# Kernel optimization log

Measured on AMD Instinct MI355X. Metric: run time of the kernel, lower is better.

Reference implementation:

```python
import jax, jax.numpy as jnp
import numpy as np

TOP_K = 2


def setup_inputs() -> dict:
    key = jax.random.key(0)
    k0, k1, k2, k3, k4 = jax.random.split(key, 5)
    B, S, H, F, E = 2, 1024, 2048, 7168, 8
    scale = 0.02
    return {
        "hidden_states": jax.random.normal(k0, (B, S, H), jnp.float32),
        "Wg": jax.random.normal(k1, (E, H), jnp.float32) * scale,
        "w1": jax.random.normal(k2, (E, F, H), jnp.float32) * scale,
        "w3": jax.random.normal(k3, (E, F, H), jnp.float32) * scale,
        "w2": jax.random.normal(k4, (E, H, F), jnp.float32) * scale,
    }


def reference(hidden_states, Wg, w1, w3, w2):
    B, S, H = hidden_states.shape
    E = Wg.shape[0]
    x = hidden_states.reshape(-1, H)                      # [T, H]
    T = x.shape[0]

    # Router: logits -> softmax (float32) -> top-k -> renormalize
    router_logits = jnp.einsum("th,eh->te", x, Wg)        # [T, E]
    probs = jax.nn.softmax(router_logits.astype(jnp.float32), axis=-1)
    top_w, top_idx = jax.lax.top_k(probs, TOP_K)          # [T, K]
    top_w = top_w / jnp.sum(top_w, axis=-1, keepdims=True)
    top_w = top_w.astype(x.dtype)

    # Combine weights: [T, E], zero for unselected experts
    combine = jnp.zeros((T, E), x.dtype).at[
        jnp.arange(T)[:, None], top_idx
    ].add(top_w)

    out = jnp.zeros((T, H), x.dtype)
    for e in range(E):
        h = jax.nn.silu(x @ w1[e].T) * (x @ w3[e].T)      # [T, F]
        out = out + (h @ w2[e].T) * combine[:, e:e + 1]   # [T, H]

    return out.reshape(B, S, H), router_logits
```

## Files before the change

### kernel.cpp

```cpp
#include <hip/hip_runtime.h>

#define T_TOK 2048
#define H_DIM 2048
#define F_DIM 7168
#define E_NUM 8
#define MAX_SLOTS 5120
#define N13 (2 * F_DIM)

typedef __attribute__((ext_vector_type(8))) _Float16 f16x8;
typedef __attribute__((ext_vector_type(4))) float    f32x4;

#define GLL(g, l) __builtin_amdgcn_global_load_lds(                          \
    (const __attribute__((address_space(1))) void*)(g),                      \
    (__attribute__((address_space(3))) void*)(l), 16, 0, 0)


__global__ __launch_bounds__(256) void cvt13_kernel(const float* __restrict__ w1,
                                                    const float* __restrict__ w3,
                                                    _Float16* __restrict__ w13h) {
    int b = blockIdx.x;
    int e = b / N13;
    int c = b - e * N13;
    int blk = c >> 6, sub = c & 63;
    int f = blk * 32 + (sub & 31);
    const float* src = (sub < 32 ? w1 : w3) + ((size_t)e * F_DIM + f) * H_DIM + threadIdx.x * 8;
    _Float16* dst = w13h + (size_t)b * H_DIM + threadIdx.x * 8;
    float4 a = *(const float4*)src;
    float4 bb = *(const float4*)(src + 4);
    f16x8 h;
    h[0]=(_Float16)a.x;  h[1]=(_Float16)a.y;  h[2]=(_Float16)a.z;  h[3]=(_Float16)a.w;
    h[4]=(_Float16)bb.x; h[5]=(_Float16)bb.y; h[6]=(_Float16)bb.z; h[7]=(_Float16)bb.w;
    *(f16x8*)dst = h;
}

__global__ __launch_bounds__(256) void cvtw_kernel(const float* __restrict__ src,
                                                   _Float16* __restrict__ dst) {
    size_t i = ((size_t)blockIdx.x * 256 + threadIdx.x) * 8;
    float4 a = *(const float4*)(src + i);
    float4 b = *(const float4*)(src + i + 4);
    f16x8 h;
    h[0]=(_Float16)a.x; h[1]=(_Float16)a.y; h[2]=(_Float16)a.z; h[3]=(_Float16)a.w;
    h[4]=(_Float16)b.x; h[5]=(_Float16)b.y; h[6]=(_Float16)b.z; h[7]=(_Float16)b.w;
    *(f16x8*)(dst + i) = h;
}


__global__ __launch_bounds__(256) void router_kernel(
    const float* __restrict__ x, const float* __restrict__ wg,
    float* __restrict__ logits_out, int* __restrict__ tk_e,
    float* __restrict__ tk_w, int* __restrict__ meta) {
    int wave = threadIdx.x >> 6;
    int lane = threadIdx.x & 63;
    int t = blockIdx.x * 4 + wave;
    const float* xr = x + (size_t)t * H_DIM;

    float xv[32];
#pragma unroll
    for (int i = 0; i < 8; i++) {
        float4 v = *(const float4*)(xr + i * 256 + lane * 4);
        xv[i*4+0] = v.x; xv[i*4+1] = v.y; xv[i*4+2] = v.z; xv[i*4+3] = v.w;
    }
    float lg[E_NUM];
#pragma unroll
    for (int e = 0; e < E_NUM; e++) {
        const float* wr = wg + (size_t)e * H_DIM;
        float acc = 0.f;
#pragma unroll
        for (int i = 0; i < 8; i++) {
            float4 v = *(const float4*)(wr + i * 256 + lane * 4);
            acc += xv[i*4+0]*v.x + xv[i*4+1]*v.y + xv[i*4+2]*v.z + xv[i*4+3]*v.w;
        }
#pragma unroll
        for (int s = 32; s > 0; s >>= 1) acc += __shfl_xor(acc, s, 64);
        lg[e] = acc;
    }
    if (lane == 0) {
        float b0 = -3e38f, b1 = -3e38f; int i0 = 0, i1 = 0;
#pragma unroll
        for (int e = 0; e < E_NUM; e++) {
            float le = lg[e];
            if (le > b0)      { b1 = b0; i1 = i0; b0 = le; i0 = e; }
            else if (le > b1) { b1 = le; i1 = e; }
        }
        float w0 = 1.f / (1.f + __expf(b1 - b0));
        float w1v = 1.f - w0;
#pragma unroll
        for (int e = 0; e < E_NUM; e++) logits_out[(size_t)t * E_NUM + e] = lg[e];
        tk_e[t*2+0] = i0; tk_w[t*2+0] = w0;
        tk_e[t*2+1] = i1; tk_w[t*2+1] = w1v;
        atomicAdd(&meta[i0], 1);
        atomicAdd(&meta[i1], 1);
    }
}

__global__ void scan_kernel(int* __restrict__ meta, int* __restrict__ slot_tok,
                            float* __restrict__ slot_w) {
    int lane = threadIdx.x;
    int cnts[E_NUM], pads[E_NUM], bases[E_NUM];
    int run = 0;
#pragma unroll
    for (int e = 0; e < E_NUM; e++) {
        cnts[e] = meta[e];
        pads[e] = (cnts[e] + 127) & ~127;
        bases[e] = run;
        run += pads[e];
    }
    if (lane < E_NUM) { meta[8 + lane] = pads[lane]; meta[16 + lane] = bases[lane]; }
    for (int e = 0; e < E_NUM; e++)
        for (int i = cnts[e] + lane; i < pads[e]; i += 64) {
            slot_tok[bases[e] + i] = 0;
            slot_w[bases[e] + i] = 0.f;
        }
}

__global__ __launch_bounds__(256) void assign_kernel(
    const int* __restrict__ tk_e, const float* __restrict__ tk_w,
    int* __restrict__ meta, int* __restrict__ slot_tok, float* __restrict__ slot_w) {
    int t = blockIdx.x * 256 + threadIdx.x;
    if (t >= T_TOK) return;
#pragma unroll
    for (int k = 0; k < 2; k++) {
        int e = tk_e[t*2+k];
        int pos = atomicAdd(&meta[24 + e], 1);
        int s = meta[16 + e] + pos;
        slot_tok[s] = t;
        slot_w[s] = tk_w[t*2+k];
    }
}

__global__ __launch_bounds__(512, 2) void ffn1_kernel(
    const _Float16* __restrict__ xb, const _Float16* __restrict__ w13h,
    const int* __restrict__ slot_tok, const int* __restrict__ meta,
    _Float16* __restrict__ hbuf) {
    int e = blockIdx.z;
    int cntpad = meta[8 + e];
    int mb = blockIdx.y;
    if (mb * 256 >= cntpad) return;
    int base = meta[16 + e];
    int nb = blockIdx.x;

    __shared__ _Float16 sA[2][256][64];
    __shared__ _Float16 sB[2][256][64];

    int tid  = threadIdx.x;
    int lane = tid & 63;
    int wave = tid >> 6;
    int wm = wave >> 2, wn = wave & 3;
    int w8 = wave * 8;

    int lr = lane & 15;
    int sw = lane & 7;
    int sg = lane >> 4;
    int offk0 = lr * 64 + ((sg    ) ^ sw) * 8;
    int offk1 = lr * 64 + ((sg + 4) ^ sw) * 8;

    int rsub = lane >> 3;
    int sl   = (lane & 7) ^ rsub;
    int slot0 = base + mb * 256;

    const _Float16* aG[4];
    const _Float16* bG[4];
#pragma unroll
    for (int q = 0; q < 4; q++) {
        int r = mb * 256 + q * 64 + w8 + rsub;
        int tok = (r < cntpad) ? slot_tok[base + r] : 0;
        aG[q] = xb + (size_t)tok * H_DIM + sl * 8;
        bG[q] = w13h + ((size_t)e * N13 + (size_t)nb * 256 + q * 64 + w8 + rsub) * H_DIM + sl * 8;
    }

    f32x4 zero = {0.f, 0.f, 0.f, 0.f};
    f32x4 acc[8][4];
#pragma unroll
    for (int m = 0; m < 8; m++)
#pragma unroll
        for (int n = 0; n < 4; n++) acc[m][n] = zero;

    const int NT = H_DIM / 64;
#pragma unroll
    for (int q = 0; q < 4; q++) GLL(aG[q] + 0,  &sA[0][q*64 + w8][0]);
#pragma unroll
    for (int q = 0; q < 4; q++) GLL(bG[q] + 0,  &sB[0][q*64 + w8][0]);
#pragma unroll
    for (int q = 0; q < 4; q++) GLL(aG[q] + 64, &sA[1][q*64 + w8][0]);
#pragma unroll
    for (int q = 0; q < 4; q++) GLL(bG[q] + 64, &sB[1][q*64 + w8][0]);

    for (int t = 0; t < NT; ++t) {
        if (t < NT - 1) asm volatile("s_waitcnt vmcnt(8)" ::: "memory");
        else            asm volatile("s_waitcnt vmcnt(0)" ::: "memory");
        __builtin_amdgcn_sched_barrier(0);
        __builtin_amdgcn_s_barrier();
        __builtin_amdgcn_sched_barrier(0);
        int bd = t & 1;
        const _Float16* Ab = &sA[bd][wm * 128][0];
        const _Float16* Bb = &sB[bd][wn * 64][0];
        f16x8 bf[2][4];
#pragma unroll
        for (int n = 0; n < 4; n++) {
            bf[0][n] = *(const f16x8*)(const void*)(Bb + n * 1024 + offk0);
            bf[1][n] = *(const f16x8*)(const void*)(Bb + n * 1024 + offk1);
        }
        __builtin_amdgcn_s_setprio(1);
#pragma unroll
        for (int m = 0; m < 8; m++) {
            f16x8 a0 = *(const f16x8*)(const void*)(Ab + m * 1024 + offk0);
            f16x8 a1 = *(const f16x8*)(const void*)(Ab + m * 1024 + offk1);
#pragma unroll
            for (int n = 0; n < 4; n++) {
                acc[m][n] = __builtin_amdgcn_mfma_f32_16x16x32_f16(a0, bf[0][n], acc[m][n], 0, 0, 0);
                acc[m][n] = __builtin_amdgcn_mfma_f32_16x16x32_f16(a1, bf[1][n], acc[m][n], 0, 0, 0);
            }
        }
        __builtin_amdgcn_s_setprio(0);
        __builtin_amdgcn_sched_barrier(0);
        __builtin_amdgcn_s_barrier();
        __builtin_amdgcn_sched_barrier(0);
        if (t + 2 < NT) {
            int k2 = (t + 2) * 64;
#pragma unroll
            for (int q = 0; q < 4; q++) GLL(aG[q] + k2, &sA[bd][q*64 + w8][0]);
#pragma unroll
            for (int q = 0; q < 4; q++) GLL(bG[q] + k2, &sB[bd][q*64 + w8][0]);
        }
    }

    int row_e0 = mb * 256 + wm * 128;
    int fb = nb * 128 + wn * 32;
#pragma unroll
    for (int m = 0; m < 8; m++) {
#pragma unroll
        for (int j = 0; j < 4; j++) {
            int re = row_e0 + m * 16 + (lane >> 4) * 4 + j;
            if (re < cntpad) {
                size_t srow = (size_t)(base + re) * F_DIM;
#pragma unroll
                for (int n = 0; n < 2; n++) {
                    float a1 = acc[m][n][j], a3 = acc[m][n + 2][j];
                    float hv = a1 * a3 / (1.f + __expf(-a1));
                    hbuf[srow + fb + n * 16 + lr] = (_Float16)hv;
                }
            }
        }
    }
}

__global__ __launch_bounds__(512, 2) void ffn2_kernel(
    const _Float16* __restrict__ hbuf, const _Float16* __restrict__ w2h,
    const int* __restrict__ slot_tok, const float* __restrict__ slot_w,
    const int* __restrict__ meta, float* __restrict__ out) {
    int e = blockIdx.z;
    int cntpad = meta[8 + e];
    int mb = blockIdx.y;
    if (mb * 128 >= cntpad) return;
    int base = meta[16 + e];
    int nb = blockIdx.x;

    __shared__ _Float16 sA[2][128][64];
    __shared__ _Float16 sB[2][256][64];

    int tid  = threadIdx.x;
    int lane = tid & 63;
    int wave = tid >> 6;
    int wm = wave >> 2, wn = wave & 3;
    int w8 = wave * 8;

    int lr = lane & 15;
    int sw = lane & 7;
    int sg = lane >> 4;
    int offk0 = lr * 64 + ((sg    ) ^ sw) * 8;
    int offk1 = lr * 64 + ((sg + 4) ^ sw) * 8;

    int rsub = lane >> 3;
    int sl   = (lane & 7) ^ rsub;
    int slot0 = base + mb * 128;

    const _Float16* aG[2];
    const _Float16* bG[4];
#pragma unroll
    for (int q = 0; q < 2; q++)
        aG[q] = hbuf + (size_t)(slot0 + q * 64 + w8 + rsub) * F_DIM + sl * 8;
#pragma unroll
    for (int q = 0; q < 4; q++)
        bG[q] = w2h + ((size_t)e * H_DIM + (size_t)nb * 256 + q * 64 + w8 + rsub) * F_DIM + sl * 8;

    f32x4 zero = {0.f, 0.f, 0.f, 0.f};
    f32x4 acc[4][4];
#pragma unroll
    for (int m = 0; m < 4; m++)
#pragma unroll
        for (int n = 0; n < 4; n++) acc[m][n] = zero;

    const int NT = F_DIM / 64;
#pragma unroll
    for (int q = 0; q < 2; q++) GLL(aG[q] + 0,  &sA[0][q*64 + w8][0]);
#pragma unroll
    for (int q = 0; q < 4; q++) GLL(bG[q] + 0,  &sB[0][q*64 + w8][0]);
#pragma unroll
    for (int q = 0; q < 2; q++) GLL(aG[q] + 64, &sA[1][q*64 + w8][0]);
#pragma unroll
    for (int q = 0; q < 4; q++) GLL(bG[q] + 64, &sB[1][q*64 + w8][0]);

    for (int t = 0; t < NT; ++t) {
        if (t < NT - 1) asm volatile("s_waitcnt vmcnt(6)" ::: "memory");
        else            asm volatile("s_waitcnt vmcnt(0)" ::: "memory");
        __builtin_amdgcn_sched_barrier(0);
        __builtin_amdgcn_s_barrier();
        __builtin_amdgcn_sched_barrier(0);
        int bd = t & 1;
        const _Float16* Ab = &sA[bd][wm * 64][0];
        const _Float16* Bb = &sB[bd][wn * 64][0];
        f16x8 bf[2][4];
#pragma unroll
        for (int n = 0; n < 4; n++) {
            bf[0][n] = *(const f16x8*)(const void*)(Bb + n * 1024 + offk0);
            bf[1][n] = *(const f16x8*)(const void*)(Bb + n * 1024 + offk1);
        }
        __builtin_amdgcn_s_setprio(1);
#pragma unroll
        for (int m = 0; m < 4; m++) {
            f16x8 a0 = *(const f16x8*)(const void*)(Ab + m * 1024 + offk0);
            f16x8 a1 = *(const f16x8*)(const void*)(Ab + m * 1024 + offk1);
#pragma unroll
            for (int n = 0; n < 4; n++) {
                acc[m][n] = __builtin_amdgcn_mfma_f32_16x16x32_f16(a0, bf[0][n], acc[m][n], 0, 0, 0);
                acc[m][n] = __builtin_amdgcn_mfma_f32_16x16x32_f16(a1, bf[1][n], acc[m][n], 0, 0, 0);
            }
        }
        __builtin_amdgcn_s_setprio(0);
        __builtin_amdgcn_sched_barrier(0);
        __builtin_amdgcn_s_barrier();
        __builtin_amdgcn_sched_barrier(0);
        if (t + 2 < NT) {
            int k2 = (t + 2) * 64;
#pragma unroll
            for (int q = 0; q < 2; q++) GLL(aG[q] + k2, &sA[bd][q*64 + w8][0]);
#pragma unroll
            for (int q = 0; q < 4; q++) GLL(bG[q] + k2, &sB[bd][q*64 + w8][0]);
        }
    }

    int row0 = mb * 128 + wm * 64;
    int col0 = nb * 256 + wn * 64;
#pragma unroll
    for (int m = 0; m < 4; m++) {
        int rb = row0 + m * 16 + (lane >> 4) * 4;
        int toks[4]; float wts[4];
#pragma unroll
        for (int j = 0; j < 4; j++) {
            int s = base + rb + j;
            toks[j] = slot_tok[s];
            wts[j]  = slot_w[s];
        }
#pragma unroll
        for (int n = 0; n < 4; n++) {
            int col = col0 + n * 16 + lr;
            f32x4 v = acc[m][n];
#pragma unroll
            for (int j = 0; j < 4; j++)
                atomicAdd(&out[(size_t)toks[j] * H_DIM + col], v[j] * wts[j]);
        }
    }
}

extern "C" void kernel_launch(void* const* d_in, const int* in_sizes, int n_in,
                              void* d_out, int out_size, void* d_ws, size_t ws_size,
                              hipStream_t stream) {
    const float* x  = (const float*)d_in[0];
    const float* wg = (const float*)d_in[1];
    const float* w1 = (const float*)d_in[2];
    const float* w3 = (const float*)d_in[3];
    const float* w2 = (const float*)d_in[4];
    float* out = (float*)d_out;
    float* logits = out + (size_t)T_TOK * H_DIM;

    const size_t WELEM = (size_t)E_NUM * F_DIM * H_DIM;

    char* ws = (char*)d_ws;
    _Float16* w13h = (_Float16*)ws;
    _Float16* w2h  = w13h + 2 * WELEM;
    _Float16* hbuf = w2h + WELEM;
    _Float16* xb   = hbuf + (size_t)MAX_SLOTS * F_DIM;
    char* p = (char*)(xb + (size_t)T_TOK * H_DIM);
    int*   slot_tok = (int*)p;   p += MAX_SLOTS * 4;
    float* slot_w   = (float*)p; p += MAX_SLOTS * 4;
    int*   tk_e     = (int*)p;   p += T_TOK * 2 * 4;
    float* tk_w     = (float*)p; p += T_TOK * 2 * 4;
    int*   meta     = (int*)p;

    hipMemsetAsync(d_out, 0, (size_t)out_size * sizeof(float), stream);
    hipMemsetAsync(meta, 0, 32 * sizeof(int), stream);

    cvt13_kernel<<<dim3(E_NUM * N13), 256, 0, stream>>>(w1, w3, w13h);
    cvtw_kernel<<<dim3(WELEM / (256 * 8)), 256, 0, stream>>>(w2, w2h);
    cvtw_kernel<<<dim3((size_t)T_TOK * H_DIM / (256 * 8)), 256, 0, stream>>>(x, xb);

    router_kernel<<<dim3(T_TOK / 4), 256, 0, stream>>>(x, wg, logits, tk_e, tk_w, meta);
    scan_kernel<<<dim3(1), 64, 0, stream>>>(meta, slot_tok, slot_w);
    assign_kernel<<<dim3(T_TOK / 256), 256, 0, stream>>>(tk_e, tk_w, meta, slot_tok, slot_w);

    ffn1_kernel<<<dim3(N13 / 256, 8, E_NUM), 512, 0, stream>>>(xb, w13h, slot_tok, meta, hbuf);
    ffn2_kernel<<<dim3(H_DIM / 256, 16, E_NUM), 512, 0, stream>>>(hbuf, w2h, slot_tok, slot_w, meta, out);
}
```

Baseline: 1.292 ms.

## Fuse fp32 weight conversion into FFN GEMM loads, drop separate conversion passes

Removes the standalone kernels that convert w1/w3/w2 to fp16 in workspace. The FFN GEMMs now read fp32 weights straight from global memory into registers, convert them, and write them to swizzled shared memory, so the weight-conversion round trip through HBM goes away. Tiles shrink to 128x128 with 256-thread blocks, single-buffered shared memory, and register prefetch of the next weight tile. The cost is that each weight tile is read in fp32 by every M-block of an expert, which doubles weight bytes per read, and the kernels lose the earlier double-buffered LDS pipeline.

```diff
diff --git a/kernel.cpp b/kernel.cpp
--- a/kernel.cpp
+++ b/kernel.cpp
@@ -5,7 +5,6 @@
 #define F_DIM 7168
 #define E_NUM 8
 #define MAX_SLOTS 5120
-#define N13 (2 * F_DIM)
 
 typedef __attribute__((ext_vector_type(8))) _Float16 f16x8;
 typedef __attribute__((ext_vector_type(4))) float    f32x4;
@@ -15,25 +14,7 @@
     (__attribute__((address_space(3))) void*)(l), 16, 0, 0)
 
 
-__global__ __launch_bounds__(256) void cvt13_kernel(const float* __restrict__ w1,
-                                                    const float* __restrict__ w3,
-                                                    _Float16* __restrict__ w13h) {
-    int b = blockIdx.x;
-    int e = b / N13;
-    int c = b - e * N13;
-    int blk = c >> 6, sub = c & 63;
-    int f = blk * 32 + (sub & 31);
-    const float* src = (sub < 32 ? w1 : w3) + ((size_t)e * F_DIM + f) * H_DIM + threadIdx.x * 8;
-    _Float16* dst = w13h + (size_t)b * H_DIM + threadIdx.x * 8;
-    float4 a = *(const float4*)src;
-    float4 bb = *(const float4*)(src + 4);
-    f16x8 h;
-    h[0]=(_Float16)a.x;  h[1]=(_Float16)a.y;  h[2]=(_Float16)a.z;  h[3]=(_Float16)a.w;
-    h[4]=(_Float16)bb.x; h[5]=(_Float16)bb.y; h[6]=(_Float16)bb.z; h[7]=(_Float16)bb.w;
-    *(f16x8*)dst = h;
-}
-
-__global__ __launch_bounds__(256) void cvtw_kernel(const float* __restrict__ src,
+__global__ __launch_bounds__(256) void cvtx_kernel(const float* __restrict__ src,
                                                    _Float16* __restrict__ dst) {
     size_t i = ((size_t)blockIdx.x * 256 + threadIdx.x) * 8;
     float4 a = *(const float4*)(src + i);
@@ -44,7 +25,6 @@
     *(f16x8*)(dst + i) = h;
 }
 
-
 __global__ __launch_bounds__(256) void router_kernel(
     const float* __restrict__ x, const float* __restrict__ wg,
     float* __restrict__ logits_out, int* __restrict__ tk_e,
@@ -128,124 +108,125 @@
     }
 }
 
-__global__ __launch_bounds__(512, 2) void ffn1_kernel(
-    const _Float16* __restrict__ xb, const _Float16* __restrict__ w13h,
-    const int* __restrict__ slot_tok, const int* __restrict__ meta,
-    _Float16* __restrict__ hbuf) {
+__global__ __launch_bounds__(256, 4) void ffn1_kernel(
+    const _Float16* __restrict__ xb, const float* __restrict__ w1,
+    const float* __restrict__ w3, const int* __restrict__ slot_tok,
+    const int* __restrict__ meta, _Float16* __restrict__ hbuf) {
     int e = blockIdx.z;
     int cntpad = meta[8 + e];
     int mb = blockIdx.y;
-    if (mb * 256 >= cntpad) return;
+    if (mb * 128 >= cntpad) return;
     int base = meta[16 + e];
     int nb = blockIdx.x;
 
-    __shared__ _Float16 sA[2][256][64];
-    __shared__ _Float16 sB[2][256][64];
+    __shared__ _Float16 sA[128][64];
+    __shared__ _Float16 sB[128][64];
+    char* sAc = (char*)&sA[0][0];
+    char* sBc = (char*)&sB[0][0];
 
     int tid  = threadIdx.x;
     int lane = tid & 63;
     int wave = tid >> 6;
-    int wm = wave >> 2, wn = wave & 3;
-    int w8 = wave * 8;
-
     int lr = lane & 15;
-    int sw = lane & 7;
     int sg = lane >> 4;
-    int offk0 = lr * 64 + ((sg    ) ^ sw) * 8;
-    int offk1 = lr * 64 + ((sg + 4) ^ sw) * 8;
+    int sw7 = lane & 7;
+    int bro0 = ((sg    ) ^ sw7) * 16;
+    int bro1 = ((sg + 4) ^ sw7) * 16;
 
     int rsub = lane >> 3;
-    int sl   = (lane & 7) ^ rsub;
-    int slot0 = base + mb * 256;
-
+    int sl = (lane & 7) ^ rsub;
     const _Float16* aG[4];
-    const _Float16* bG[4];
 #pragma unroll
     for (int q = 0; q < 4; q++) {
-        int r = mb * 256 + q * 64 + w8 + rsub;
-        int tok = (r < cntpad) ? slot_tok[base + r] : 0;
+        int row = mb * 128 + wave * 32 + q * 8 + rsub;
+        int tok = slot_tok[base + row];
         aG[q] = xb + (size_t)tok * H_DIM + sl * 8;
-        bG[q] = w13h + ((size_t)e * N13 + (size_t)nb * 256 + q * 64 + w8 + rsub) * H_DIM + sl * 8;
-    }
+    }
+
+    int brow = wave * 32 + (lane >> 1);
+    const float* wsel = (brow < 64) ? w1 : w3;
+    const float* bsrc = wsel + ((size_t)e * F_DIM + (size_t)nb * 64 + (brow & 63)) * H_DIM
+                        + (lane & 1) * 32;
+    int bwr[4];
+#pragma unroll
+    for (int q = 0; q < 4; q++)
+        bwr[q] = brow * 128 + ((((lane & 1) * 4 + q) ^ (brow & 7)) * 16);
 
     f32x4 zero = {0.f, 0.f, 0.f, 0.f};
-    f32x4 acc[8][4];
-#pragma unroll
-    for (int m = 0; m < 8; m++)
-#pragma unroll
-        for (int n = 0; n < 4; n++) acc[m][n] = zero;
+    f32x4 acc[2][8];
+#pragma unroll
+    for (int m = 0; m < 2; m++)
+#pragma unroll
+        for (int n = 0; n < 8; n++) acc[m][n] = zero;
 
     const int NT = H_DIM / 64;
-#pragma unroll
-    for (int q = 0; q < 4; q++) GLL(aG[q] + 0,  &sA[0][q*64 + w8][0]);
-#pragma unroll
-    for (int q = 0; q < 4; q++) GLL(bG[q] + 0,  &sB[0][q*64 + w8][0]);
-#pragma unroll
-    for (int q = 0; q < 4; q++) GLL(aG[q] + 64, &sA[1][q*64 + w8][0]);
-#pragma unroll
-    for (int q = 0; q < 4; q++) GLL(bG[q] + 64, &sB[1][q*64 + w8][0]);
+    float4 br[8];
+#pragma unroll
+    for (int q = 0; q < 8; q++) br[q] = *(const float4*)(bsrc + q * 4);
 
     for (int t = 0; t < NT; ++t) {
-        if (t < NT - 1) asm volatile("s_waitcnt vmcnt(8)" ::: "memory");
-        else            asm volatile("s_waitcnt vmcnt(0)" ::: "memory");
+        int k = t * 64;
         __builtin_amdgcn_sched_barrier(0);
         __builtin_amdgcn_s_barrier();
         __builtin_amdgcn_sched_barrier(0);
-        int bd = t & 1;
-        const _Float16* Ab = &sA[bd][wm * 128][0];
-        const _Float16* Bb = &sB[bd][wn * 64][0];
-        f16x8 bf[2][4];
-#pragma unroll
-        for (int n = 0; n < 4; n++) {
-            bf[0][n] = *(const f16x8*)(const void*)(Bb + n * 1024 + offk0);
-            bf[1][n] = *(const f16x8*)(const void*)(Bb + n * 1024 + offk1);
-        }
+#pragma unroll
+        for (int q = 0; q < 4; q++) {
+            float4 a = br[2*q], b = br[2*q+1];
+            f16x8 p;
+            p[0]=(_Float16)a.x; p[1]=(_Float16)a.y; p[2]=(_Float16)a.z; p[3]=(_Float16)a.w;
+            p[4]=(_Float16)b.x; p[5]=(_Float16)b.y; p[6]=(_Float16)b.z; p[7]=(_Float16)b.w;
+            *(f16x8*)(sBc + bwr[q]) = p;
+        }
+#pragma unroll
+        for (int q = 0; q < 4; q++) GLL(aG[q] + k, &sA[wave * 32 + q * 8][0]);
+        if (t + 1 < NT) {
+#pragma unroll
+            for (int q = 0; q < 8; q++) br[q] = *(const float4*)(bsrc + k + 64 + q * 4);
+            asm volatile("s_waitcnt vmcnt(8) lgkmcnt(0)" ::: "memory");
+        } else {
+            asm volatile("s_waitcnt vmcnt(0) lgkmcnt(0)" ::: "memory");
+        }
+        __builtin_amdgcn_sched_barrier(0);
+        __builtin_amdgcn_s_barrier();
+        __builtin_amdgcn_sched_barrier(0);
         __builtin_amdgcn_s_setprio(1);
 #pragma unroll
-        for (int m = 0; m < 8; m++) {
-            f16x8 a0 = *(const f16x8*)(const void*)(Ab + m * 1024 + offk0);
-            f16x8 a1 = *(const f16x8*)(const void*)(Ab + m * 1024 + offk1);
+        for (int ks = 0; ks < 2; ks++) {
+            int bro = ks ? bro1 : bro0;
+            f16x8 bf[8];
+#pragma unroll
+            for (int n = 0; n < 8; n++)
+                bf[n] = *(const f16x8*)(sBc + (n * 16 + lr) * 128 + bro);
+#pragma unroll
+            for (int m = 0; m < 2; m++) {
+                f16x8 av = *(const f16x8*)(sAc + (wave * 32 + m * 16 + lr) * 128 + bro);
+#pragma unroll
+                for (int n = 0; n < 8; n++)
+                    acc[m][n] = __builtin_amdgcn_mfma_f32_16x16x32_f16(av, bf[n], acc[m][n], 0, 0, 0);
+            }
+        }
+        __builtin_amdgcn_s_setprio(0);
+    }
+
+    int fb = nb * 64;
+#pragma unroll
+    for (int m = 0; m < 2; m++) {
+#pragma unroll
+        for (int j = 0; j < 4; j++) {
+            int row = mb * 128 + wave * 32 + m * 16 + sg * 4 + j;
+            size_t srow = (size_t)(base + row) * F_DIM;
 #pragma unroll
             for (int n = 0; n < 4; n++) {
-                acc[m][n] = __builtin_amdgcn_mfma_f32_16x16x32_f16(a0, bf[0][n], acc[m][n], 0, 0, 0);
-                acc[m][n] = __builtin_amdgcn_mfma_f32_16x16x32_f16(a1, bf[1][n], acc[m][n], 0, 0, 0);
+                float a1 = acc[m][n][j], a3 = acc[m][n + 4][j];
+                float hv = a1 * a3 / (1.f + __expf(-a1));
+                hbuf[srow + fb + n * 16 + lr] = (_Float16)hv;
             }
         }
-        __builtin_amdgcn_s_setprio(0);
-        __builtin_amdgcn_sched_barrier(0);
-        __builtin_amdgcn_s_barrier();
-        __builtin_amdgcn_sched_barrier(0);
-        if (t + 2 < NT) {
-            int k2 = (t + 2) * 64;
-#pragma unroll
-            for (int q = 0; q < 4; q++) GLL(aG[q] + k2, &sA[bd][q*64 + w8][0]);
-#pragma unroll
-            for (int q = 0; q < 4; q++) GLL(bG[q] + k2, &sB[bd][q*64 + w8][0]);
-        }
-    }
-
-    int row_e0 = mb * 256 + wm * 128;
-    int fb = nb * 128 + wn * 32;
-#pragma unroll
-    for (int m = 0; m < 8; m++) {
-#pragma unroll
-        for (int j = 0; j < 4; j++) {
-            int re = row_e0 + m * 16 + (lane >> 4) * 4 + j;
-            if (re < cntpad) {
-                size_t srow = (size_t)(base + re) * F_DIM;
-#pragma unroll
-                for (int n = 0; n < 2; n++) {
-                    float a1 = acc[m][n][j], a3 = acc[m][n + 2][j];
-                    float hv = a1 * a3 / (1.f + __expf(-a1));
-                    hbuf[srow + fb + n * 16 + lr] = (_Float16)hv;
-                }
-            }
-        }
-    }
-}
-
-__global__ __launch_bounds__(512, 2) void ffn2_kernel(
-    const _Float16* __restrict__ hbuf, const _Float16* __restrict__ w2h,
+    }
+}
+
+__global__ __launch_bounds__(256, 4) void ffn2_kernel(
+    const _Float16* __restrict__ hbuf, const float* __restrict__ w2,
     const int* __restrict__ slot_tok, const float* __restrict__ slot_w,
     const int* __restrict__ meta, float* __restrict__ out) {
     int e = blockIdx.z;
@@ -255,33 +236,36 @@
     int base = meta[16 + e];
     int nb = blockIdx.x;
 
-    __shared__ _Float16 sA[2][128][64];
-    __shared__ _Float16 sB[2][256][64];
+    __shared__ _Float16 sA[128][64];
+    __shared__ _Float16 sB[128][64];
+    char* sAc = (char*)&sA[0][0];
+    char* sBc = (char*)&sB[0][0];
 
     int tid  = threadIdx.x;
     int lane = tid & 63;
     int wave = tid >> 6;
-    int wm = wave >> 2, wn = wave & 3;
-    int w8 = wave * 8;
-
+    int wm = wave >> 1, wn = wave & 1;
     int lr = lane & 15;
-    int sw = lane & 7;
     int sg = lane >> 4;
-    int offk0 = lr * 64 + ((sg    ) ^ sw) * 8;
-    int offk1 = lr * 64 + ((sg + 4) ^ sw) * 8;
+    int sw7 = lane & 7;
+    int bro0 = ((sg    ) ^ sw7) * 16;
+    int bro1 = ((sg + 4) ^ sw7) * 16;
 
     int rsub = lane >> 3;
-    int sl   = (lane & 7) ^ rsub;
+    int sl = (lane & 7) ^ rsub;
     int slot0 = base + mb * 128;
-
-    const _Float16* aG[2];
-    const _Float16* bG[4];
-#pragma unroll
-    for (int q = 0; q < 2; q++)
-        aG[q] = hbuf + (size_t)(slot0 + q * 64 + w8 + rsub) * F_DIM + sl * 8;
+    const _Float16* aG[4];
 #pragma unroll
     for (int q = 0; q < 4; q++)
-        bG[q] = w2h + ((size_t)e * H_DIM + (size_t)nb * 256 + q * 64 + w8 + rsub) * F_DIM + sl * 8;
+        aG[q] = hbuf + (size_t)(slot0 + wave * 32 + q * 8 + rsub) * F_DIM + sl * 8;
+
+    int brow = wave * 32 + (lane >> 1);
+    const float* bsrc = w2 + ((size_t)e * H_DIM + (size_t)nb * 128 + brow) * F_DIM
+                        + (lane & 1) * 32;
+    int bwr[4];
+#pragma unroll
+    for (int q = 0; q < 4; q++)
+        bwr[q] = brow * 128 + ((((lane & 1) * 4 + q) ^ (brow & 7)) * 16);
 
     f32x4 zero = {0.f, 0.f, 0.f, 0.f};
     f32x4 acc[4][4];
@@ -291,59 +275,59 @@
         for (int n = 0; n < 4; n++) acc[m][n] = zero;
 
     const int NT = F_DIM / 64;
-#pragma unroll
-    for (int q = 0; q < 2; q++) GLL(aG[q] + 0,  &sA[0][q*64 + w8][0]);
-#pragma unroll
-    for (int q = 0; q < 4; q++) GLL(bG[q] + 0,  &sB[0][q*64 + w8][0]);
-#pragma unroll
-    for (int q = 0; q < 2; q++) GLL(aG[q] + 64, &sA[1][q*64 + w8][0]);
-#pragma unroll
-    for (int q = 0; q < 4; q++) GLL(bG[q] + 64, &sB[1][q*64 + w8][0]);
+    float4 br[8];
+#pragma unroll
+    for (int q = 0; q < 8; q++) br[q] = *(const float4*)(bsrc + q * 4);
 
     for (int t = 0; t < NT; ++t) {
-        if (t < NT - 1) asm volatile("s_waitcnt vmcnt(6)" ::: "memory");
-        else            asm volatile("s_waitcnt vmcnt(0)" ::: "memory");
+        int k = t * 64;
         __builtin_amdgcn_sched_barrier(0);
         __builtin_amdgcn_s_barrier();
         __builtin_amdgcn_sched_barrier(0);
-        int bd = t & 1;
-        const _Float16* Ab = &sA[bd][wm * 64][0];
-        const _Float16* Bb = &sB[bd][wn * 64][0];
-        f16x8 bf[2][4];
-#pragma unroll
-        for (int n = 0; n < 4; n++) {
-            bf[0][n] = *(const f16x8*)(const void*)(Bb + n * 1024 + offk0);
-            bf[1][n] = *(const f16x8*)(const void*)(Bb + n * 1024 + offk1);
-        }
+#pragma unroll
+        for (int q = 0; q < 4; q++) {
+            float4 a = br[2*q], b = br[2*q+1];
+            f16x8 p;
+            p[0]=(_Float16)a.x; p[1]=(_Float16)a.y; p[2]=(_Float16)a.z; p[3]=(_Float16)a.w;
+            p[4]=(_Float16)b.x; p[5]=(_Float16)b.y; p[6]=(_Float16)b.z; p[7]=(_Float16)b.w;
+            *(f16x8*)(sBc + bwr[q]) = p;
+        }
+#pragma unroll
+        for (int q = 0; q < 4; q++) GLL(aG[q] + k, &sA[wave * 32 + q * 8][0]);
+        if (t + 1 < NT) {
+#pragma unroll
+            for (int q = 0; q < 8; q++) br[q] = *(const float4*)(bsrc + k + 64 + q * 4);
+            asm volatile("s_waitcnt vmcnt(8) lgkmcnt(0)" ::: "memory");
+        } else {
+            asm volatile("s_waitcnt vmcnt(0) lgkmcnt(0)" ::: "memory");
+        }
+        __builtin_amdgcn_sched_barrier(0);
+        __builtin_amdgcn_s_barrier();
+        __builtin_amdgcn_sched_barrier(0);
         __builtin_amdgcn_s_setprio(1);
 #pragma unroll
-        for (int m = 0; m < 4; m++) {
-            f16x8 a0 = *(const f16x8*)(const void*)(Ab + m * 1024 + offk0);
-            f16x8 a1 = *(const f16x8*)(const void*)(Ab + m * 1024 + offk1);
-#pragma unroll
-            for (int n = 0; n < 4; n++) {
-                acc[m][n] = __builtin_amdgcn_mfma_f32_16x16x32_f16(a0, bf[0][n], acc[m][n], 0, 0, 0);
-                acc[m][n] = __builtin_amdgcn_mfma_f32_16x16x32_f16(a1, bf[1][n], acc[m][n], 0, 0, 0);
+        for (int ks = 0; ks < 2; ks++) {
+            int bro = ks ? bro1 : bro0;
+            f16x8 bf[4];
+#pragma unroll
+            for (int n = 0; n < 4; n++)
+                bf[n] = *(const f16x8*)(sBc + ((wn * 64 + n * 16 + lr) * 128) + bro);
+#pragma unroll
+            for (int m = 0; m < 4; m++) {
+                f16x8 av = *(const f16x8*)(sAc + ((wm * 64 + m * 16 + lr) * 128) + bro);
+#pragma unroll
+                for (int n = 0; n < 4; n++)
+                    acc[m][n] = __builtin_amdgcn_mfma_f32_16x16x32_f16(av, bf[n], acc[m][n], 0, 0, 0);
             }
         }
         __builtin_amdgcn_s_setprio(0);
-        __builtin_amdgcn_sched_barrier(0);
-        __builtin_amdgcn_s_barrier();
-        __builtin_amdgcn_sched_barrier(0);
-        if (t + 2 < NT) {
-            int k2 = (t + 2) * 64;
-#pragma unroll
-            for (int q = 0; q < 2; q++) GLL(aG[q] + k2, &sA[bd][q*64 + w8][0]);
-#pragma unroll
-            for (int q = 0; q < 4; q++) GLL(bG[q] + k2, &sB[bd][q*64 + w8][0]);
-        }
     }
 
     int row0 = mb * 128 + wm * 64;
-    int col0 = nb * 256 + wn * 64;
+    int col0 = nb * 128 + wn * 64;
 #pragma unroll
     for (int m = 0; m < 4; m++) {
-        int rb = row0 + m * 16 + (lane >> 4) * 4;
+        int rb = row0 + m * 16 + sg * 4;
         int toks[4]; float wts[4];
 #pragma unroll
         for (int j = 0; j < 4; j++) {
@@ -373,12 +357,8 @@
     float* out = (float*)d_out;
     float* logits = out + (size_t)T_TOK * H_DIM;
 
-    const size_t WELEM = (size_t)E_NUM * F_DIM * H_DIM;
-
     char* ws = (char*)d_ws;
-    _Float16* w13h = (_Float16*)ws;
-    _Float16* w2h  = w13h + 2 * WELEM;
-    _Float16* hbuf = w2h + WELEM;
+    _Float16* hbuf = (_Float16*)ws;
     _Float16* xb   = hbuf + (size_t)MAX_SLOTS * F_DIM;
     char* p = (char*)(xb + (size_t)T_TOK * H_DIM);
     int*   slot_tok = (int*)p;   p += MAX_SLOTS * 4;
@@ -390,14 +370,11 @@
     hipMemsetAsync(d_out, 0, (size_t)out_size * sizeof(float), stream);
     hipMemsetAsync(meta, 0, 32 * sizeof(int), stream);
 
-    cvt13_kernel<<<dim3(E_NUM * N13), 256, 0, stream>>>(w1, w3, w13h);
-    cvtw_kernel<<<dim3(WELEM / (256 * 8)), 256, 0, stream>>>(w2, w2h);
-    cvtw_kernel<<<dim3((size_t)T_TOK * H_DIM / (256 * 8)), 256, 0, stream>>>(x, xb);
-
+    cvtx_kernel<<<dim3((size_t)T_TOK * H_DIM / (256 * 8)), 256, 0, stream>>>(x, xb);
     router_kernel<<<dim3(T_TOK / 4), 256, 0, stream>>>(x, wg, logits, tk_e, tk_w, meta);
     scan_kernel<<<dim3(1), 64, 0, stream>>>(meta, slot_tok, slot_w);
     assign_kernel<<<dim3(T_TOK / 256), 256, 0, stream>>>(tk_e, tk_w, meta, slot_tok, slot_w);
 
-    ffn1_kernel<<<dim3(N13 / 256, 8, E_NUM), 512, 0, stream>>>(xb, w13h, slot_tok, meta, hbuf);
-    ffn2_kernel<<<dim3(H_DIM / 256, 16, E_NUM), 512, 0, stream>>>(hbuf, w2h, slot_tok, slot_w, meta, out);
-}
+    ffn1_kernel<<<dim3(F_DIM / 64, 16, E_NUM), 256, 0, stream>>>(xb, w1, w3, slot_tok, meta, hbuf);
+    ffn2_kernel<<<dim3(H_DIM / 128, 16, E_NUM), 256, 0, stream>>>(hbuf, w2, slot_tok, slot_w, meta, out);
+}
```

Result: slower. 4.829 ms (+273.9%).

## Triple-buffer LDS and split K-steps into interleaved load/MFMA phases in FFN GEMMs

Applied to the files above, without the earlier changes.

Both FFN GEMM kernels move from double to triple-buffered LDS and split each 64-wide K tile into two half-steps. Global-to-LDS loads for tile t+2 are spread across the two half-steps, interleaved with LDS reads and MFMA bursts. FFN1 also shrinks its M tile from 256 to 128 rows, doubling the grid's M blocks and halving accumulator registers. The cost is extra barriers per iteration and more LDS per block (about 144KB), which can limit how many blocks fit on a CU.

```diff
diff --git a/kernel.cpp b/kernel.cpp
--- a/kernel.cpp
+++ b/kernel.cpp
@@ -135,110 +135,131 @@
     int e = blockIdx.z;
     int cntpad = meta[8 + e];
     int mb = blockIdx.y;
-    if (mb * 256 >= cntpad) return;
+    if (mb * 128 >= cntpad) return;
     int base = meta[16 + e];
     int nb = blockIdx.x;
 
-    __shared__ _Float16 sA[2][256][64];
-    __shared__ _Float16 sB[2][256][64];
+    __shared__ _Float16 sA[3][128][64];
+    __shared__ _Float16 sB[3][256][64];
 
     int tid  = threadIdx.x;
     int lane = tid & 63;
     int wave = tid >> 6;
     int wm = wave >> 2, wn = wave & 3;
     int w8 = wave * 8;
-
     int lr = lane & 15;
-    int sw = lane & 7;
     int sg = lane >> 4;
-    int offk0 = lr * 64 + ((sg    ) ^ sw) * 8;
-    int offk1 = lr * 64 + ((sg + 4) ^ sw) * 8;
+    int sw7 = lane & 7;
+    int so0 = ((sg    ) ^ sw7) * 8;
+    int so1 = ((sg + 4) ^ sw7) * 8;
+    int rb  = lr * 64;
 
     int rsub = lane >> 3;
-    int sl   = (lane & 7) ^ rsub;
-    int slot0 = base + mb * 256;
-
-    const _Float16* aG[4];
+    int sl   = sw7 ^ rsub;
+    const _Float16* aG[2];
+#pragma unroll
+    for (int q = 0; q < 2; q++) {
+        int row = q * 64 + w8 + rsub;
+        int tok = slot_tok[base + mb * 128 + row];
+        aG[q] = xb + (size_t)tok * H_DIM + sl * 8;
+    }
     const _Float16* bG[4];
 #pragma unroll
-    for (int q = 0; q < 4; q++) {
-        int r = mb * 256 + q * 64 + w8 + rsub;
-        int tok = (r < cntpad) ? slot_tok[base + r] : 0;
-        aG[q] = xb + (size_t)tok * H_DIM + sl * 8;
+    for (int q = 0; q < 4; q++)
         bG[q] = w13h + ((size_t)e * N13 + (size_t)nb * 256 + q * 64 + w8 + rsub) * H_DIM + sl * 8;
-    }
 
     f32x4 zero = {0.f, 0.f, 0.f, 0.f};
-    f32x4 acc[8][4];
-#pragma unroll
-    for (int m = 0; m < 8; m++)
+    f32x4 acc[4][4];
+#pragma unroll
+    for (int m = 0; m < 4; m++)
 #pragma unroll
         for (int n = 0; n < 4; n++) acc[m][n] = zero;
 
     const int NT = H_DIM / 64;
-#pragma unroll
-    for (int q = 0; q < 4; q++) GLL(aG[q] + 0,  &sA[0][q*64 + w8][0]);
-#pragma unroll
-    for (int q = 0; q < 4; q++) GLL(bG[q] + 0,  &sB[0][q*64 + w8][0]);
-#pragma unroll
-    for (int q = 0; q < 4; q++) GLL(aG[q] + 64, &sA[1][q*64 + w8][0]);
-#pragma unroll
-    for (int q = 0; q < 4; q++) GLL(bG[q] + 64, &sB[1][q*64 + w8][0]);
+
+#pragma unroll
+    for (int t0 = 0; t0 < 2; t0++) {
+        int k = t0 * 64;
+        GLL(aG[0] + k, &sA[t0][w8][0]);
+        GLL(aG[1] + k, &sA[t0][64 + w8][0]);
+#pragma unroll
+        for (int q = 0; q < 4; q++) GLL(bG[q] + k, &sB[t0][q * 64 + w8][0]);
+    }
+    asm volatile("s_waitcnt vmcnt(6)" ::: "memory");
+    __builtin_amdgcn_sched_barrier(0);
+    __builtin_amdgcn_s_barrier();
+    __builtin_amdgcn_sched_barrier(0);
 
     for (int t = 0; t < NT; ++t) {
-        if (t < NT - 1) asm volatile("s_waitcnt vmcnt(8)" ::: "memory");
+        int r  = t % 3;
+        int r2 = (t + 2) % 3;
+        int k2 = (t + 2) * 64;
+        const _Float16* Ab = &sA[r][wm * 64][0];
+        const _Float16* Bb = &sB[r][wn * 64][0];
+
+        f16x8 a0[4], b0[4];
+#pragma unroll
+        for (int n = 0; n < 4; n++) b0[n] = *(const f16x8*)(const void*)(Bb + n * 1024 + rb + so0);
+#pragma unroll
+        for (int m = 0; m < 4; m++) a0[m] = *(const f16x8*)(const void*)(Ab + m * 1024 + rb + so0);
+        if (t + 2 < NT) {
+            GLL(aG[0] + k2, &sA[r2][w8][0]);
+            GLL(aG[1] + k2, &sA[r2][64 + w8][0]);
+            GLL(bG[0] + k2, &sB[r2][w8][0]);
+        }
+        __builtin_amdgcn_sched_barrier(0);
+        __builtin_amdgcn_s_barrier();
+        __builtin_amdgcn_sched_barrier(0);
+        __builtin_amdgcn_s_setprio(1);
+#pragma unroll
+        for (int m = 0; m < 4; m++)
+#pragma unroll
+            for (int n = 0; n < 4; n++)
+                acc[m][n] = __builtin_amdgcn_mfma_f32_16x16x32_f16(a0[m], b0[n], acc[m][n], 0, 0, 0);
+        __builtin_amdgcn_s_setprio(0);
+        __builtin_amdgcn_sched_barrier(0);
+        __builtin_amdgcn_s_barrier();
+        __builtin_amdgcn_sched_barrier(0);
+
+        f16x8 a1[4], b1[4];
+#pragma unroll
+        for (int n = 0; n < 4; n++) b1[n] = *(const f16x8*)(const void*)(Bb + n * 1024 + rb + so1);
+#pragma unroll
+        for (int m = 0; m < 4; m++) a1[m] = *(const f16x8*)(const void*)(Ab + m * 1024 + rb + so1);
+        if (t + 2 < NT) {
+            GLL(bG[1] + k2, &sB[r2][64 + w8][0]);
+            GLL(bG[2] + k2, &sB[r2][128 + w8][0]);
+            GLL(bG[3] + k2, &sB[r2][192 + w8][0]);
+        }
+        if (t < NT - 2) asm volatile("s_waitcnt vmcnt(6)" ::: "memory");
         else            asm volatile("s_waitcnt vmcnt(0)" ::: "memory");
         __builtin_amdgcn_sched_barrier(0);
         __builtin_amdgcn_s_barrier();
         __builtin_amdgcn_sched_barrier(0);
-        int bd = t & 1;
-        const _Float16* Ab = &sA[bd][wm * 128][0];
-        const _Float16* Bb = &sB[bd][wn * 64][0];
-        f16x8 bf[2][4];
-#pragma unroll
-        for (int n = 0; n < 4; n++) {
-            bf[0][n] = *(const f16x8*)(const void*)(Bb + n * 1024 + offk0);
-            bf[1][n] = *(const f16x8*)(const void*)(Bb + n * 1024 + offk1);
-        }
         __builtin_amdgcn_s_setprio(1);
 #pragma unroll
-        for (int m = 0; m < 8; m++) {
-            f16x8 a0 = *(const f16x8*)(const void*)(Ab + m * 1024 + offk0);
-            f16x8 a1 = *(const f16x8*)(const void*)(Ab + m * 1024 + offk1);
-#pragma unroll
-            for (int n = 0; n < 4; n++) {
-                acc[m][n] = __builtin_amdgcn_mfma_f32_16x16x32_f16(a0, bf[0][n], acc[m][n], 0, 0, 0);
-                acc[m][n] = __builtin_amdgcn_mfma_f32_16x16x32_f16(a1, bf[1][n], acc[m][n], 0, 0, 0);
-            }
-        }
+        for (int m = 0; m < 4; m++)
+#pragma unroll
+            for (int n = 0; n < 4; n++)
+                acc[m][n] = __builtin_amdgcn_mfma_f32_16x16x32_f16(a1[m], b1[n], acc[m][n], 0, 0, 0);
         __builtin_amdgcn_s_setprio(0);
         __builtin_amdgcn_sched_barrier(0);
         __builtin_amdgcn_s_barrier();
         __builtin_amdgcn_sched_barrier(0);
-        if (t + 2 < NT) {
-            int k2 = (t + 2) * 64;
-#pragma unroll
-            for (int q = 0; q < 4; q++) GLL(aG[q] + k2, &sA[bd][q*64 + w8][0]);
-#pragma unroll
-            for (int q = 0; q < 4; q++) GLL(bG[q] + k2, &sB[bd][q*64 + w8][0]);
-        }
-    }
-
-    int row_e0 = mb * 256 + wm * 128;
-    int fb = nb * 128 + wn * 32;
-#pragma unroll
-    for (int m = 0; m < 8; m++) {
+    }
+
+    int fb = (nb * 4 + wn) * 32;
+#pragma unroll
+    for (int m = 0; m < 4; m++) {
 #pragma unroll
         for (int j = 0; j < 4; j++) {
-            int re = row_e0 + m * 16 + (lane >> 4) * 4 + j;
-            if (re < cntpad) {
-                size_t srow = (size_t)(base + re) * F_DIM;
-#pragma unroll
-                for (int n = 0; n < 2; n++) {
-                    float a1 = acc[m][n][j], a3 = acc[m][n + 2][j];
-                    float hv = a1 * a3 / (1.f + __expf(-a1));
-                    hbuf[srow + fb + n * 16 + lr] = (_Float16)hv;
-                }
+            int re = mb * 128 + wm * 64 + m * 16 + sg * 4 + j;
+            size_t srow = (size_t)(base + re) * F_DIM;
+#pragma unroll
+            for (int n = 0; n < 2; n++) {
+                float a1v = acc[m][n][j], a3v = acc[m][n + 2][j];
+                float hv = a1v * a3v / (1.f + __expf(-a1v));
+                hbuf[srow + fb + n * 16 + lr] = (_Float16)hv;
             }
         }
     }
@@ -255,30 +276,28 @@
     int base = meta[16 + e];
     int nb = blockIdx.x;
 
-    __shared__ _Float16 sA[2][128][64];
-    __shared__ _Float16 sB[2][256][64];
+    __shared__ _Float16 sA[3][128][64];
+    __shared__ _Float16 sB[3][256][64];
 
     int tid  = threadIdx.x;
     int lane = tid & 63;
     int wave = tid >> 6;
     int wm = wave >> 2, wn = wave & 3;
     int w8 = wave * 8;
-
     int lr = lane & 15;
-    int sw = lane & 7;
     int sg = lane >> 4;
-    int offk0 = lr * 64 + ((sg    ) ^ sw) * 8;
-    int offk1 = lr * 64 + ((sg + 4) ^ sw) * 8;
+    int sw7 = lane & 7;
+    int so0 = ((sg    ) ^ sw7) * 8;
+    int so1 = ((sg + 4) ^ sw7) * 8;
+    int rb  = lr * 64;
 
     int rsub = lane >> 3;
-    int sl   = (lane & 7) ^ rsub;
-    int slot0 = base + mb * 128;
-
+    int sl   = sw7 ^ rsub;
     const _Float16* aG[2];
+#pragma unroll
+    for (int q = 0; q < 2; q++)
+        aG[q] = hbuf + (size_t)(base + mb * 128 + q * 64 + w8 + rsub) * F_DIM + sl * 8;
     const _Float16* bG[4];
-#pragma unroll
-    for (int q = 0; q < 2; q++)
-        aG[q] = hbuf + (size_t)(slot0 + q * 64 + w8 + rsub) * F_DIM + sl * 8;
 #pragma unroll
     for (int q = 0; q < 4; q++)
         bG[q] = w2h + ((size_t)e * H_DIM + (size_t)nb * 256 + q * 64 + w8 + rsub) * F_DIM + sl * 8;
@@ -291,63 +310,87 @@
         for (int n = 0; n < 4; n++) acc[m][n] = zero;
 
     const int NT = F_DIM / 64;
-#pragma unroll
-    for (int q = 0; q < 2; q++) GLL(aG[q] + 0,  &sA[0][q*64 + w8][0]);
-#pragma unroll
-    for (int q = 0; q < 4; q++) GLL(bG[q] + 0,  &sB[0][q*64 + w8][0]);
-#pragma unroll
-    for (int q = 0; q < 2; q++) GLL(aG[q] + 64, &sA[1][q*64 + w8][0]);
-#pragma unroll
-    for (int q = 0; q < 4; q++) GLL(bG[q] + 64, &sB[1][q*64 + w8][0]);
+
+#pragma unroll
+    for (int t0 = 0; t0 < 2; t0++) {
+        int k = t0 * 64;
+        GLL(aG[0] + k, &sA[t0][w8][0]);
+        GLL(aG[1] + k, &sA[t0][64 + w8][0]);
+#pragma unroll
+        for (int q = 0; q < 4; q++) GLL(bG[q] + k, &sB[t0][q * 64 + w8][0]);
+    }
+    asm volatile("s_waitcnt vmcnt(6)" ::: "memory");
+    __builtin_amdgcn_sched_barrier(0);
+    __builtin_amdgcn_s_barrier();
+    __builtin_amdgcn_sched_barrier(0);
 
     for (int t = 0; t < NT; ++t) {
-        if (t < NT - 1) asm volatile("s_waitcnt vmcnt(6)" ::: "memory");
+        int r  = t % 3;
+        int r2 = (t + 2) % 3;
+        int k2 = (t + 2) * 64;
+        const _Float16* Ab = &sA[r][wm * 64][0];
+        const _Float16* Bb = &sB[r][wn * 64][0];
+
+        f16x8 a0[4], b0[4];
+#pragma unroll
+        for (int n = 0; n < 4; n++) b0[n] = *(const f16x8*)(const void*)(Bb + n * 1024 + rb + so0);
+#pragma unroll
+        for (int m = 0; m < 4; m++) a0[m] = *(const f16x8*)(const void*)(Ab + m * 1024 + rb + so0);
+        if (t + 2 < NT) {
+            GLL(aG[0] + k2, &sA[r2][w8][0]);
+            GLL(aG[1] + k2, &sA[r2][64 + w8][0]);
+            GLL(bG[0] + k2, &sB[r2][w8][0]);
+        }
+        __builtin_amdgcn_sched_barrier(0);
+        __builtin_amdgcn_s_barrier();
+        __builtin_amdgcn_sched_barrier(0);
+        __builtin_amdgcn_s_setprio(1);
+#pragma unroll
+        for (int m = 0; m < 4; m++)
+#pragma unroll
+            for (int n = 0; n < 4; n++)
+                acc[m][n] = __builtin_amdgcn_mfma_f32_16x16x32_f16(a0[m], b0[n], acc[m][n], 0, 0, 0);
+        __builtin_amdgcn_s_setprio(0);
+        __builtin_amdgcn_sched_barrier(0);
+        __builtin_amdgcn_s_barrier();
+        __builtin_amdgcn_sched_barrier(0);
+
+        f16x8 a1[4], b1[4];
+#pragma unroll
+        for (int n = 0; n < 4; n++) b1[n] = *(const f16x8*)(const void*)(Bb + n * 1024 + rb + so1);
+#pragma unroll
+        for (int m = 0; m < 4; m++) a1[m] = *(const f16x8*)(const void*)(Ab + m * 1024 + rb + so1);
+        if (t + 2 < NT) {
+            GLL(bG[1] + k2, &sB[r2][64 + w8][0]);
+            GLL(bG[2] + k2, &sB[r2][128 + w8][0]);
+            GLL(bG[3] + k2, &sB[r2][192 + w8][0]);
+        }
+        if (t < NT - 2) asm volatile("s_waitcnt vmcnt(6)" ::: "memory");
         else            asm volatile("s_waitcnt vmcnt(0)" ::: "memory");
         __builtin_amdgcn_sched_barrier(0);
         __builtin_amdgcn_s_barrier();
         __builtin_amdgcn_sched_barrier(0);
-        int bd = t & 1;
-        const _Float16* Ab = &sA[bd][wm * 64][0];
-        const _Float16* Bb = &sB[bd][wn * 64][0];
-        f16x8 bf[2][4];
-#pragma unroll
-        for (int n = 0; n < 4; n++) {
-            bf[0][n] = *(const f16x8*)(const void*)(Bb + n * 1024 + offk0);
-            bf[1][n] = *(const f16x8*)(const void*)(Bb + n * 1024 + offk1);
-        }
         __builtin_amdgcn_s_setprio(1);
 #pragma unroll
-        for (int m = 0; m < 4; m++) {
-            f16x8 a0 = *(const f16x8*)(const void*)(Ab + m * 1024 + offk0);
-            f16x8 a1 = *(const f16x8*)(const void*)(Ab + m * 1024 + offk1);
-#pragma unroll
-            for (int n = 0; n < 4; n++) {
-                acc[m][n] = __builtin_amdgcn_mfma_f32_16x16x32_f16(a0, bf[0][n], acc[m][n], 0, 0, 0);
-                acc[m][n] = __builtin_amdgcn_mfma_f32_16x16x32_f16(a1, bf[1][n], acc[m][n], 0, 0, 0);
-            }
-        }
+        for (int m = 0; m < 4; m++)
+#pragma unroll
+            for (int n = 0; n < 4; n++)
+                acc[m][n] = __builtin_amdgcn_mfma_f32_16x16x32_f16(a1[m], b1[n], acc[m][n], 0, 0, 0);
         __builtin_amdgcn_s_setprio(0);
         __builtin_amdgcn_sched_barrier(0);
         __builtin_amdgcn_s_barrier();
         __builtin_amdgcn_sched_barrier(0);
-        if (t + 2 < NT) {
-            int k2 = (t + 2) * 64;
-#pragma unroll
-            for (int q = 0; q < 2; q++) GLL(aG[q] + k2, &sA[bd][q*64 + w8][0]);
-#pragma unroll
-            for (int q = 0; q < 4; q++) GLL(bG[q] + k2, &sB[bd][q*64 + w8][0]);
-        }
     }
 
     int row0 = mb * 128 + wm * 64;
     int col0 = nb * 256 + wn * 64;
 #pragma unroll
     for (int m = 0; m < 4; m++) {
-        int rb = row0 + m * 16 + (lane >> 4) * 4;
+        int rbw = row0 + m * 16 + sg * 4;
         int toks[4]; float wts[4];
 #pragma unroll
         for (int j = 0; j < 4; j++) {
-            int s = base + rb + j;
+            int s = base + rbw + j;
             toks[j] = slot_tok[s];
             wts[j]  = slot_w[s];
         }
@@ -398,6 +441,6 @@
     scan_kernel<<<dim3(1), 64, 0, stream>>>(meta, slot_tok, slot_w);
     assign_kernel<<<dim3(T_TOK / 256), 256, 0, stream>>>(tk_e, tk_w, meta, slot_tok, slot_w);
 
-    ffn1_kernel<<<dim3(N13 / 256, 8, E_NUM), 512, 0, stream>>>(xb, w13h, slot_tok, meta, hbuf);
+    ffn1_kernel<<<dim3(N13 / 256, 16, E_NUM), 512, 0, stream>>>(xb, w13h, slot_tok, meta, hbuf);
     ffn2_kernel<<<dim3(H_DIM / 256, 16, E_NUM), 512, 0, stream>>>(hbuf, w2h, slot_tok, slot_w, meta, out);
 }
```

New measurement: 1.203 ms. 6.8% less time.
